# Kernel tuning notes

Measured on AMD Instinct MI355X. Metric: run time of the kernel, lower is better.

The kernel has to match this reference:

```python
import jax, jax.numpy as jnp
import numpy as np


def setup_inputs() -> dict:
    key = jax.random.key(0)
    ks = jax.random.split(key, 7)
    B, T, K, H, A = 32, 32, 196, 512, 512
    # Xavier-normal-ish scale for square 512x512 linears
    s = float(np.sqrt(2.0 / (H + A)))
    return {
        "att_feats": jax.random.normal(ks[0], (B, K, H), jnp.float32),
        "hiddens": jax.random.normal(ks[1], (B, T, H), jnp.float32),
        "sentinel": jax.random.normal(ks[2], (B, T, H), jnp.float32),
        "Wv": jax.random.normal(ks[3], (H, A), jnp.float32) * s,
        "Wg": jax.random.normal(ks[4], (H, A), jnp.float32) * s,
        "Ws": jax.random.normal(ks[5], (H, A), jnp.float32) * s,
        "wh": jax.random.normal(ks[6], (A,), jnp.float32) * s,
    }


def reference(att_feats, hiddens, sentinel, Wv, Wg, Ws, wh):
    # Dropout treated as identity (eval mode / deterministic reference).
    cv = jnp.einsum("bkh,ha->bka", att_feats, Wv)          # [B,K,A]
    cg = jnp.einsum("bth,ha->bta", hiddens, Wg)            # [B,T,A]
    # Broadcast additive attention: [B,T,K,A]
    content_v = cv[:, None, :, :] + cg[:, :, None, :]
    z_t = jnp.einsum("btka,a->btk", jnp.tanh(content_v), wh)  # [B,T,K]
    alpha_t = jax.nn.softmax(z_t, axis=-1)                    # [B,T,K]
    c_t = jnp.einsum("btk,bkh->bth", alpha_t, att_feats)      # [B,T,H]
    # Sentinel branch
    content_s = jnp.einsum("bth,ha->bta", sentinel, Ws) + cg  # [B,T,A]
    z_ext = jnp.einsum("bta,a->bt", jnp.tanh(content_s), wh)[..., None]  # [B,T,1]
    extended = jnp.concatenate([z_t, z_ext], axis=2)          # [B,T,K+1]
    alpha_hat = jax.nn.softmax(extended, axis=-1)
    beta_t = alpha_hat[:, :, -1:]                             # [B,T,1]
    c_hat_t = beta_t * sentinel + (1.0 - beta_t) * c_t        # [B,T,H]
    return (c_hat_t, alpha_t, beta_t)
```

## Files before the change

### kernel.cpp

```cpp
#include <hip/hip_runtime.h>
#include <hip/hip_bf16.h>
#include <math.h>

#define HDIM 512
#define ADIM 512
#define BATCH 32
#define TDIM 32
#define KDIM 196
#define MROWS 8320

typedef short short8 __attribute__((ext_vector_type(8)));
typedef float floatx4 __attribute__((ext_vector_type(4)));

__device__ __forceinline__ float tanh_fast(float x) {
    float e = __expf(2.0f * x);
    return 1.0f - 2.0f * __builtin_amdgcn_rcpf(e + 1.0f);
}

__device__ __forceinline__ void gl_lds16(const __hip_bfloat16* g, __hip_bfloat16* l) {
    __builtin_amdgcn_global_load_lds(
        (const __attribute__((address_space(1))) unsigned int*)(const void*)g,
        (__attribute__((address_space(3))) unsigned int*)(void*)l, 16, 0, 0);
}

__global__ __launch_bounds__(256) void convA(const float* __restrict__ att,
                                             const float* __restrict__ hid,
                                             const float* __restrict__ sen,
                                             __hip_bfloat16* __restrict__ ahi,
                                             __hip_bfloat16* __restrict__ alo) {
    const int idx = blockIdx.x * 256 + threadIdx.x;
    const int row = idx >> 7;
    float4 v;
    if (row < 6272)      v = ((const float4*)att)[idx];
    else if (row < 7296) v = ((const float4*)hid)[idx - 6272 * 128];
    else                 v = ((const float4*)sen)[idx - 7296 * 128];
    float x[4] = {v.x, v.y, v.z, v.w};
    union { __hip_bfloat16 b[4]; uint2 u; } H, L;
    #pragma unroll
    for (int i = 0; i < 4; ++i) {
        H.b[i] = __float2bfloat16(x[i]);
        L.b[i] = __float2bfloat16(x[i] - __bfloat162float(H.b[i]));
    }
    ((uint2*)ahi)[idx] = H.u;
    ((uint2*)alo)[idx] = L.u;
}

__global__ __launch_bounds__(256) void convB(const float* __restrict__ Wv,
                                             const float* __restrict__ Wg,
                                             const float* __restrict__ Ws,
                                             __hip_bfloat16* __restrict__ bthi,
                                             __hip_bfloat16* __restrict__ btlo) {
    __shared__ float tile[64][65];
    const int tid = threadIdx.x;
    const float* src = blockIdx.z == 0 ? Wv : (blockIdx.z == 1 ? Wg : Ws);
    const int k0 = blockIdx.x * 64, n0 = blockIdx.y * 64;
    #pragma unroll
    for (int i = 0; i < 16; ++i) {
        int k = (tid >> 6) * 16 + i;
        int n = tid & 63;
        tile[k][n] = src[(size_t)(k0 + k) * 512 + n0 + n];
    }
    __syncthreads();
    const size_t obase = (size_t)blockIdx.z * 262144;
    #pragma unroll
    for (int i = 0; i < 16; ++i) {
        int n = (tid >> 6) * 16 + i;
        int k = tid & 63;
        float x = tile[k][n];
        __hip_bfloat16 h = __float2bfloat16(x);
        __hip_bfloat16 l = __float2bfloat16(x - __bfloat162float(h));
        size_t o = obase + (size_t)(n0 + n) * 512 + k0 + k;
        bthi[o] = h;
        btlo[o] = l;
    }
}

__global__ __launch_bounds__(256) void gemm_bf16x3(
        const __hip_bfloat16* __restrict__ Ahi, const __hip_bfloat16* __restrict__ Alo,
        const __hip_bfloat16* __restrict__ Bthi, const __hip_bfloat16* __restrict__ Btlo,
        float* __restrict__ C) {
    __shared__ __hip_bfloat16 smem[12288];

    const int tid  = threadIdx.x;
    const int lane = tid & 63;
    const int wave = tid >> 6;
    const int wm = wave >> 1;
    const int wn = wave & 1;
    const int row0 = blockIdx.x * 64;
    const int col0 = blockIdx.y * 128;
    const int seg = (row0 < 6272) ? 0 : ((row0 < 7296) ? 1 : 2);
    const __hip_bfloat16* Bh = Bthi + (size_t)seg * 262144;
    const __hip_bfloat16* Bl = Btlo + (size_t)seg * 262144;

    floatx4 acc[2][4];
    #pragma unroll
    for (int i = 0; i < 2; ++i)
        #pragma unroll
        for (int j = 0; j < 4; ++j)
            acc[i][j] = (floatx4){0.f, 0.f, 0.f, 0.f};

    const int kq8 = (lane >> 4) << 3;

    for (int k0 = 0; k0 < 512; k0 += 32) {
        #pragma unroll
        for (int s = 0; s < 6; ++s) {
            int u = tid + (s << 8);
            __hip_bfloat16* ldst = smem + u * 8;
            const __hip_bfloat16* gsrc;
            if (u < 256)        gsrc = Ahi + (size_t)(row0 + (u >> 2)) * 512 + k0 + ((u & 3) << 3);
            else if (u < 512)   { int v = u - 256;  gsrc = Alo + (size_t)(row0 + (v >> 2)) * 512 + k0 + ((v & 3) << 3); }
            else if (u < 1024)  { int v = u - 512;  gsrc = Bh  + (size_t)(col0 + (v >> 2)) * 512 + k0 + ((v & 3) << 3); }
            else                { int v = u - 1024; gsrc = Bl  + (size_t)(col0 + (v >> 2)) * 512 + k0 + ((v & 3) << 3); }
            gl_lds16(gsrc, ldst);
        }
        asm volatile("s_waitcnt vmcnt(0)" ::: "memory");
        __syncthreads();

        short8 a_hi[2], a_lo[2], b_hi[4], b_lo[4];
        #pragma unroll
        for (int i = 0; i < 2; ++i) {
            int m = wm * 32 + i * 16 + (lane & 15);
            a_hi[i] = *(const short8*)(smem + m * 32 + kq8);
            a_lo[i] = *(const short8*)(smem + 2048 + m * 32 + kq8);
        }
        #pragma unroll
        for (int j = 0; j < 4; ++j) {
            int n = wn * 64 + j * 16 + (lane & 15);
            b_hi[j] = *(const short8*)(smem + 4096 + n * 32 + kq8);
            b_lo[j] = *(const short8*)(smem + 8192 + n * 32 + kq8);
        }

        #pragma unroll
        for (int i = 0; i < 2; ++i)
            #pragma unroll
            for (int j = 0; j < 4; ++j) {
                acc[i][j] = __builtin_amdgcn_mfma_f32_16x16x32_bf16(a_hi[i], b_hi[j], acc[i][j], 0, 0, 0);
                acc[i][j] = __builtin_amdgcn_mfma_f32_16x16x32_bf16(a_hi[i], b_lo[j], acc[i][j], 0, 0, 0);
                acc[i][j] = __builtin_amdgcn_mfma_f32_16x16x32_bf16(a_lo[i], b_hi[j], acc[i][j], 0, 0, 0);
            }
        __syncthreads();
    }

    #pragma unroll
    for (int i = 0; i < 2; ++i) {
        #pragma unroll
        for (int r = 0; r < 4; ++r) {
            int row = row0 + wm * 32 + i * 16 + ((lane >> 4) << 2) + r;
            float* cp = C + (size_t)row * 512 + col0 + wn * 64 + (lane & 15);
            #pragma unroll
            for (int j = 0; j < 4; ++j) cp[j * 16] = acc[i][j][r];
        }
    }
}

__global__ __launch_bounds__(256) void gemm_f32(const float* __restrict__ Amat,
                                                const float* __restrict__ Bmat,
                                                float* __restrict__ Cmat) {
    __shared__ float As[16][64 + 4];
    __shared__ float Bs[16][64];
    const int tid = threadIdx.x;
    const int tx = tid & 15;
    const int ty = tid >> 4;
    const int row0 = blockIdx.x * 64;
    const int col0 = blockIdx.y * 64;
    float acc[4][4] = {};
    for (int k0 = 0; k0 < HDIM; k0 += 16) {
        #pragma unroll
        for (int i = 0; i < 4; ++i) {
            int idx = tid + i * 256;
            As[idx & 15][idx >> 4] = Amat[(size_t)(row0 + (idx >> 4)) * HDIM + k0 + (idx & 15)];
        }
        #pragma unroll
        for (int i = 0; i < 4; ++i) {
            int idx = tid + i * 256;
            Bs[idx >> 6][idx & 63] = Bmat[(size_t)(k0 + (idx >> 6)) * ADIM + col0 + (idx & 63)];
        }
        __syncthreads();
        #pragma unroll
        for (int k = 0; k < 16; ++k) {
            float4 a4 = *(const float4*)&As[k][ty * 4];
            float4 b4 = *(const float4*)&Bs[k][tx * 4];
            float a[4] = {a4.x, a4.y, a4.z, a4.w};
            float b[4] = {b4.x, b4.y, b4.z, b4.w};
            #pragma unroll
            for (int i = 0; i < 4; ++i)
                #pragma unroll
                for (int j = 0; j < 4; ++j)
                    acc[i][j] += a[i] * b[j];
        }
        __syncthreads();
    }
    #pragma unroll
    for (int i = 0; i < 4; ++i) {
        size_t r = (size_t)(row0 + ty * 4 + i) * ADIM + col0 + tx * 4;
        #pragma unroll
        for (int j = 0; j < 4; ++j) Cmat[r + j] = acc[i][j];
    }
}

#define ZKC 16
__global__ __launch_bounds__(512) void z_kernel(const float* __restrict__ cv,
                                                const float* __restrict__ cg,
                                                const float* __restrict__ cs,
                                                const float* __restrict__ wh,
                                                float* __restrict__ z_t,
                                                float* __restrict__ z_ext) {
    __shared__ float cvs[ZKC][ADIM];

    const int b    = blockIdx.x;
    const int tg   = blockIdx.y;
    const int ks   = blockIdx.z;
    const int wave = threadIdx.x >> 6;
    const int lane = threadIdx.x & 63;
    const int t    = tg * 8 + wave;
    const int k_begin = ks * 49;

    const float4* cgv = (const float4*)(cg + ((size_t)b * TDIM + t) * ADIM);
    float4 cg0 = cgv[lane];
    float4 cg1 = cgv[64 + lane];
    const float4* whv = (const float4*)wh;
    float4 wh0 = whv[lane];
    float4 wh1 = whv[64 + lane];

    const float* cvb = cv + (size_t)b * KDIM * ADIM;

    for (int kc = 0; kc < 49; kc += ZKC) {
        int nk = min(ZKC, 49 - kc);
        __syncthreads();
        const float4* src = (const float4*)(cvb + (size_t)(k_begin + kc) * ADIM);
        for (int i = threadIdx.x; i < nk * 128; i += 512)
            ((float4*)cvs)[i] = src[i];
        __syncthreads();

        for (int kk = 0; kk < nk; ++kk) {
            float4 v0 = ((const float4*)&cvs[kk][0])[lane];
            float4 v1 = ((const float4*)&cvs[kk][0])[64 + lane];
            float p;
            p  = wh0.x * tanh_fast(v0.x + cg0.x);
            p += wh0.y * tanh_fast(v0.y + cg0.y);
            p += wh0.z * tanh_fast(v0.z + cg0.z);
            p += wh0.w * tanh_fast(v0.w + cg0.w);
            p += wh1.x * tanh_fast(v1.x + cg1.x);
            p += wh1.y * tanh_fast(v1.y + cg1.y);
            p += wh1.z * tanh_fast(v1.z + cg1.z);
            p += wh1.w * tanh_fast(v1.w + cg1.w);
            #pragma unroll
            for (int off = 32; off; off >>= 1) p += __shfl_xor(p, off, 64);
            if (lane == 0)
                z_t[((size_t)b * TDIM + t) * KDIM + k_begin + kc + kk] = p;
        }
    }

    if (ks == 0) {
        const float4* csv = (const float4*)(cs + ((size_t)b * TDIM + t) * ADIM);
        float4 s0 = csv[lane];
        float4 s1 = csv[64 + lane];
        float p;
        p  = wh0.x * tanh_fast(s0.x + cg0.x);
        p += wh0.y * tanh_fast(s0.y + cg0.y);
        p += wh0.z * tanh_fast(s0.z + cg0.z);
        p += wh0.w * tanh_fast(s0.w + cg0.w);
        p += wh1.x * tanh_fast(s1.x + cg1.x);
        p += wh1.y * tanh_fast(s1.y + cg1.y);
        p += wh1.z * tanh_fast(s1.z + cg1.z);
        p += wh1.w * tanh_fast(s1.w + cg1.w);
        #pragma unroll
        for (int off = 32; off; off >>= 1) p += __shfl_xor(p, off, 64);
        if (lane == 0) z_ext[b * TDIM + t] = p;
    }
}

__global__ __launch_bounds__(256) void out_kernel(const float* __restrict__ z_t,
                                                  const float* __restrict__ z_ext,
                                                  const float* __restrict__ att,
                                                  const float* __restrict__ sen,
                                                  float* __restrict__ out_chat,
                                                  float* __restrict__ out_alpha,
                                                  float* __restrict__ out_beta) {
    __shared__ float alpha_s[KDIM];
    __shared__ float red[8];

    const int t = blockIdx.x;
    const int b = blockIdx.y;
    const int tid = threadIdx.x;

    const float* zrow = z_t + ((size_t)b * TDIM + t) * KDIM;
    float z = (tid < KDIM) ? zrow[tid] : -INFINITY;

    float m = z;
    #pragma unroll
    for (int off = 32; off; off >>= 1) m = fmaxf(m, __shfl_xor(m, off, 64));
    if ((tid & 63) == 0) red[tid >> 6] = m;
    __syncthreads();
    m = fmaxf(fmaxf(red[0], red[1]), fmaxf(red[2], red[3]));

    float e = (tid < KDIM) ? __expf(z - m) : 0.0f;
    float s = e;
    #pragma unroll
    for (int off = 32; off; off >>= 1) s += __shfl_xor(s, off, 64);
    if ((tid & 63) == 0) red[4 + (tid >> 6)] = s;
    __syncthreads();
    float S = red[4] + red[5] + red[6] + red[7];

    float alpha = e / S;
    if (tid < KDIM) {
        alpha_s[tid] = alpha;
        out_alpha[((size_t)b * TDIM + t) * KDIM + tid] = alpha;
    }

    float se = z_ext[b * TDIM + t];
    float m2 = fmaxf(m, se);
    float eext = __expf(se - m2);
    float S2 = S * __expf(m - m2) + eext;
    float beta = eext / S2;
    if (tid == 0) out_beta[b * TDIM + t] = beta;
    __syncthreads();

    const float* attb = att + (size_t)b * KDIM * HDIM;
    float acc0 = 0.f, acc1 = 0.f;
    #pragma unroll 4
    for (int k = 0; k < KDIM; ++k) {
        float a = alpha_s[k];
        acc0 += a * attb[(size_t)k * HDIM + tid];
        acc1 += a * attb[(size_t)k * HDIM + tid + 256];
    }
    const float* srow = sen + ((size_t)b * TDIM + t) * HDIM;
    float om = 1.0f - beta;
    size_t o = ((size_t)b * TDIM + t) * HDIM;
    out_chat[o + tid]       = beta * srow[tid]       + om * acc0;
    out_chat[o + tid + 256] = beta * srow[tid + 256] + om * acc1;
}

extern "C" void kernel_launch(void* const* d_in, const int* in_sizes, int n_in,
                              void* d_out, int out_size, void* d_ws, size_t ws_size,
                              hipStream_t stream) {
    const float* att = (const float*)d_in[0];
    const float* hid = (const float*)d_in[1];
    const float* sen = (const float*)d_in[2];
    const float* Wv  = (const float*)d_in[3];
    const float* Wg  = (const float*)d_in[4];
    const float* Ws  = (const float*)d_in[5];
    const float* wh  = (const float*)d_in[6];

    float* out = (float*)d_out;
    float* out_chat  = out;
    float* out_alpha = out + 524288;
    float* out_beta  = out + 524288 + 200704;

    char* wsb = (char*)d_ws;
    const size_t C_BYTES  = (size_t)MROWS * 512 * 4;
    const size_t ZT_BYTES = 200704 * 4;
    const size_t ZE_BYTES = 4096;
    const size_t AH_BYTES = (size_t)MROWS * 512 * 2;
    const size_t BT_BYTES = (size_t)3 * 512 * 512 * 2;
    const size_t need = C_BYTES + ZT_BYTES + ZE_BYTES + 2 * AH_BYTES + 2 * BT_BYTES;

    float* C  = (float*)wsb;
    float* cv = C;
    float* cg = C + 6272 * 512;
    float* cs = C + 7296 * 512;
    float* zt = (float*)(wsb + C_BYTES);
    float* ze = (float*)(wsb + C_BYTES + ZT_BYTES);

    if (ws_size >= need) {
        __hip_bfloat16* ahi  = (__hip_bfloat16*)(wsb + C_BYTES + ZT_BYTES + ZE_BYTES);
        __hip_bfloat16* alo  = ahi + (size_t)MROWS * 512;
        __hip_bfloat16* bthi = alo + (size_t)MROWS * 512;
        __hip_bfloat16* btlo = bthi + (size_t)3 * 512 * 512;

        convA<<<4160, 256, 0, stream>>>(att, hid, sen, ahi, alo);
        convB<<<dim3(8, 8, 3), 256, 0, stream>>>(Wv, Wg, Ws, bthi, btlo);
        gemm_bf16x3<<<dim3(130, 4), 256, 0, stream>>>(ahi, alo, bthi, btlo, C);
    } else {
        gemm_f32<<<dim3(98, 8), 256, 0, stream>>>(att, Wv, cv);
        gemm_f32<<<dim3(16, 8), 256, 0, stream>>>(hid, Wg, cg);
        gemm_f32<<<dim3(16, 8), 256, 0, stream>>>(sen, Ws, cs);
    }

    z_kernel<<<dim3(BATCH, 4, 4), 512, 0, stream>>>(cv, cg, cs, wh, zt, ze);

    out_kernel<<<dim3(TDIM, BATCH), 256, 0, stream>>>(zt, ze, att, sen,
                                                      out_chat, out_alpha, out_beta);
}
```

Measured before the change: 166.0 us.

## Restructure z and output kernels for per-thread (t,k) work and alpha reuse

The z kernel now assigns one (t,k) pair per thread and stages chunks of cv, cg and cs in LDS. This removes the per-output 64-lane shuffle reductions. The inputs are prescaled by 2*log2(e) so tanh can use exp2 and rcp directly. The output kernel processes four timesteps per block, so each att_feats load is reused across four alpha rows, cutting global reads of att by about four times. In exchange it costs more LDS traffic per FLOP, and the grids are smaller (800 and 256 blocks), which may leave the machine under-occupied.

Result: no change. 164.9 us (-0.7%).

```diff
diff --git a/kernel.cpp b/kernel.cpp
--- a/kernel.cpp
+++ b/kernel.cpp
@@ -11,11 +11,6 @@
 
 typedef short short8 __attribute__((ext_vector_type(8)));
 typedef float floatx4 __attribute__((ext_vector_type(4)));
-
-__device__ __forceinline__ float tanh_fast(float x) {
-    float e = __expf(2.0f * x);
-    return 1.0f - 2.0f * __builtin_amdgcn_rcpf(e + 1.0f);
-}
 
 __device__ __forceinline__ void gl_lds16(const __hip_bfloat16* g, __hip_bfloat16* l) {
     __builtin_amdgcn_global_load_lds(
@@ -153,6 +148,190 @@
     }
 }
 
+#define ZSC 2.885390081777927f
+
+__global__ __launch_bounds__(256) void z_kernel(const float* __restrict__ cv,
+                                                const float* __restrict__ cg,
+                                                const float* __restrict__ cs,
+                                                const float* __restrict__ wh,
+                                                float* __restrict__ z_t,
+                                                float* __restrict__ z_ext) {
+    __shared__ float cvs[8][132];
+    __shared__ float cgs[32][132];
+    __shared__ float css[32][132];
+    __shared__ float whs[132];
+
+    const int kb   = blockIdx.x;
+    const int b    = blockIdx.y;
+    const int tid  = threadIdx.x;
+    const int wave = tid >> 6;
+    const int lane = tid & 63;
+    const int t       = tid & 31;
+    const int k_local = tid >> 5;
+    const int k       = kb * 8 + k_local;
+    const bool do_z = (k < KDIM);
+    const bool do_s = (kb == 24) && (wave == 2) && (lane < 32);
+    const bool last = (kb == 24);
+
+    const int r_st = tid >> 5;
+    const int q_st = tid & 31;
+
+    float acc = 0.f, acc2 = 0.f, acc_s = 0.f, acc_s2 = 0.f;
+
+    for (int c = 0; c < 4; ++c) {
+        const int a0 = c * 128;
+        __syncthreads();
+        {
+            int kr = kb * 8 + r_st;
+            if (kr < KDIM) {
+                float4 v = *(const float4*)(cv + ((size_t)b * KDIM + kr) * ADIM + a0 + 4 * q_st);
+                *(float4*)&cvs[r_st][4 * q_st] = make_float4(v.x * ZSC, v.y * ZSC, v.z * ZSC, v.w * ZSC);
+            }
+        }
+        #pragma unroll
+        for (int s = 0; s < 4; ++s) {
+            int idx = tid + s * 256;
+            int rr = idx >> 5, qq = idx & 31;
+            float4 v = *(const float4*)(cg + ((size_t)b * TDIM + rr) * ADIM + a0 + 4 * qq);
+            *(float4*)&cgs[rr][4 * qq] = make_float4(v.x * ZSC, v.y * ZSC, v.z * ZSC, v.w * ZSC);
+        }
+        if (last) {
+            #pragma unroll
+            for (int s = 0; s < 4; ++s) {
+                int idx = tid + s * 256;
+                int rr = idx >> 5, qq = idx & 31;
+                float4 v = *(const float4*)(cs + ((size_t)b * TDIM + rr) * ADIM + a0 + 4 * qq);
+                *(float4*)&css[rr][4 * qq] = make_float4(v.x * ZSC, v.y * ZSC, v.z * ZSC, v.w * ZSC);
+            }
+        }
+        if (tid < 32)
+            *(float4*)&whs[4 * tid] = *(const float4*)(wh + a0 + 4 * tid);
+        __syncthreads();
+
+        if (do_z) {
+            #pragma unroll 16
+            for (int q = 0; q < 32; ++q) {
+                float4 v  = *(const float4*)&cvs[k_local][4 * q];
+                float4 g  = *(const float4*)&cgs[t][4 * q];
+                float4 w4 = *(const float4*)&whs[4 * q];
+                float e0 = __builtin_amdgcn_exp2f(v.x + g.x);
+                float e1 = __builtin_amdgcn_exp2f(v.y + g.y);
+                float e2 = __builtin_amdgcn_exp2f(v.z + g.z);
+                float e3 = __builtin_amdgcn_exp2f(v.w + g.w);
+                float r0 = __builtin_amdgcn_rcpf(e0 + 1.0f);
+                float r1 = __builtin_amdgcn_rcpf(e1 + 1.0f);
+                float r2 = __builtin_amdgcn_rcpf(e2 + 1.0f);
+                float r3 = __builtin_amdgcn_rcpf(e3 + 1.0f);
+                acc  = fmaf(w4.x, fmaf(-2.0f, r0, 1.0f), acc);
+                acc2 = fmaf(w4.y, fmaf(-2.0f, r1, 1.0f), acc2);
+                acc  = fmaf(w4.z, fmaf(-2.0f, r2, 1.0f), acc);
+                acc2 = fmaf(w4.w, fmaf(-2.0f, r3, 1.0f), acc2);
+            }
+        }
+        if (do_s) {
+            #pragma unroll 16
+            for (int q = 0; q < 32; ++q) {
+                float4 v  = *(const float4*)&css[lane][4 * q];
+                float4 g  = *(const float4*)&cgs[lane][4 * q];
+                float4 w4 = *(const float4*)&whs[4 * q];
+                float e0 = __builtin_amdgcn_exp2f(v.x + g.x);
+                float e1 = __builtin_amdgcn_exp2f(v.y + g.y);
+                float e2 = __builtin_amdgcn_exp2f(v.z + g.z);
+                float e3 = __builtin_amdgcn_exp2f(v.w + g.w);
+                float r0 = __builtin_amdgcn_rcpf(e0 + 1.0f);
+                float r1 = __builtin_amdgcn_rcpf(e1 + 1.0f);
+                float r2 = __builtin_amdgcn_rcpf(e2 + 1.0f);
+                float r3 = __builtin_amdgcn_rcpf(e3 + 1.0f);
+                acc_s  = fmaf(w4.x, fmaf(-2.0f, r0, 1.0f), acc_s);
+                acc_s2 = fmaf(w4.y, fmaf(-2.0f, r1, 1.0f), acc_s2);
+                acc_s  = fmaf(w4.z, fmaf(-2.0f, r2, 1.0f), acc_s);
+                acc_s2 = fmaf(w4.w, fmaf(-2.0f, r3, 1.0f), acc_s2);
+            }
+        }
+    }
+
+    if (do_z) z_t[((size_t)b * TDIM + t) * KDIM + k] = acc + acc2;
+    if (do_s) z_ext[b * TDIM + lane] = acc_s + acc_s2;
+}
+
+__global__ __launch_bounds__(256) void out_kernel(const float* __restrict__ z_t,
+                                                  const float* __restrict__ z_ext,
+                                                  const float* __restrict__ att,
+                                                  const float* __restrict__ sen,
+                                                  float* __restrict__ out_chat,
+                                                  float* __restrict__ out_alpha,
+                                                  float* __restrict__ out_beta) {
+    __shared__ float alpha_s[4][200];
+    __shared__ float beta_s[4];
+
+    const int tg = blockIdx.x;
+    const int b  = blockIdx.y;
+    const int tid  = threadIdx.x;
+    const int wave = tid >> 6;
+    const int lane = tid & 63;
+    const int t = tg * 4 + wave;
+
+    const float* zrow = z_t + ((size_t)b * TDIM + t) * KDIM;
+    float z0 = zrow[lane];
+    float z1 = zrow[lane + 64];
+    float z2 = zrow[lane + 128];
+    float z3 = (lane < 4) ? zrow[lane + 192] : -INFINITY;
+
+    float m = fmaxf(fmaxf(z0, z1), fmaxf(z2, z3));
+    #pragma unroll
+    for (int off = 32; off; off >>= 1) m = fmaxf(m, __shfl_xor(m, off, 64));
+
+    float e0 = __expf(z0 - m), e1 = __expf(z1 - m);
+    float e2 = __expf(z2 - m), e3 = (lane < 4) ? __expf(z3 - m) : 0.0f;
+    float s = e0 + e1 + e2 + e3;
+    #pragma unroll
+    for (int off = 32; off; off >>= 1) s += __shfl_xor(s, off, 64);
+
+    float invS = 1.0f / s;
+    float a0 = e0 * invS, a1 = e1 * invS, a2 = e2 * invS, a3 = e3 * invS;
+
+    float* arow = out_alpha + ((size_t)b * TDIM + t) * KDIM;
+    alpha_s[wave][lane] = a0;        arow[lane] = a0;
+    alpha_s[wave][lane + 64] = a1;   arow[lane + 64] = a1;
+    alpha_s[wave][lane + 128] = a2;  arow[lane + 128] = a2;
+    if (lane < 4) { alpha_s[wave][lane + 192] = a3; arow[lane + 192] = a3; }
+
+    if (lane == 0) {
+        float se = z_ext[b * TDIM + t];
+        float m2 = fmaxf(m, se);
+        float eext = __expf(se - m2);
+        float S2 = s * __expf(m - m2) + eext;
+        float beta = eext / S2;
+        beta_s[wave] = beta;
+        out_beta[b * TDIM + t] = beta;
+    }
+    __syncthreads();
+
+    const float* attb = att + (size_t)b * KDIM * HDIM;
+    float acc[4][2] = {};
+    #pragma unroll 4
+    for (int k = 0; k < KDIM; ++k) {
+        float av0 = attb[(size_t)k * HDIM + tid];
+        float av1 = attb[(size_t)k * HDIM + tid + 256];
+        #pragma unroll
+        for (int w = 0; w < 4; ++w) {
+            float a = alpha_s[w][k];
+            acc[w][0] = fmaf(a, av0, acc[w][0]);
+            acc[w][1] = fmaf(a, av1, acc[w][1]);
+        }
+    }
+
+    #pragma unroll
+    for (int w = 0; w < 4; ++w) {
+        int tt = tg * 4 + w;
+        float beta = beta_s[w];
+        float om = 1.0f - beta;
+        size_t o = ((size_t)b * TDIM + tt) * HDIM;
+        out_chat[o + tid]       = fmaf(beta, sen[o + tid],       om * acc[w][0]);
+        out_chat[o + tid + 256] = fmaf(beta, sen[o + tid + 256], om * acc[w][1]);
+    }
+}
+
 __global__ __launch_bounds__(256) void gemm_f32(const float* __restrict__ Amat,
                                                 const float* __restrict__ Bmat,
                                                 float* __restrict__ Cmat) {
@@ -198,139 +377,6 @@
     }
 }
 
-#define ZKC 16
-__global__ __launch_bounds__(512) void z_kernel(const float* __restrict__ cv,
-                                                const float* __restrict__ cg,
-                                                const float* __restrict__ cs,
-                                                const float* __restrict__ wh,
-                                                float* __restrict__ z_t,
-                                                float* __restrict__ z_ext) {
-    __shared__ float cvs[ZKC][ADIM];
-
-    const int b    = blockIdx.x;
-    const int tg   = blockIdx.y;
-    const int ks   = blockIdx.z;
-    const int wave = threadIdx.x >> 6;
-    const int lane = threadIdx.x & 63;
-    const int t    = tg * 8 + wave;
-    const int k_begin = ks * 49;
-
-    const float4* cgv = (const float4*)(cg + ((size_t)b * TDIM + t) * ADIM);
-    float4 cg0 = cgv[lane];
-    float4 cg1 = cgv[64 + lane];
-    const float4* whv = (const float4*)wh;
-    float4 wh0 = whv[lane];
-    float4 wh1 = whv[64 + lane];
-
-    const float* cvb = cv + (size_t)b * KDIM * ADIM;
-
-    for (int kc = 0; kc < 49; kc += ZKC) {
-        int nk = min(ZKC, 49 - kc);
-        __syncthreads();
-        const float4* src = (const float4*)(cvb + (size_t)(k_begin + kc) * ADIM);
-        for (int i = threadIdx.x; i < nk * 128; i += 512)
-            ((float4*)cvs)[i] = src[i];
-        __syncthreads();
-
-        for (int kk = 0; kk < nk; ++kk) {
-            float4 v0 = ((const float4*)&cvs[kk][0])[lane];
-            float4 v1 = ((const float4*)&cvs[kk][0])[64 + lane];
-            float p;
-            p  = wh0.x * tanh_fast(v0.x + cg0.x);
-            p += wh0.y * tanh_fast(v0.y + cg0.y);
-            p += wh0.z * tanh_fast(v0.z + cg0.z);
-            p += wh0.w * tanh_fast(v0.w + cg0.w);
-            p += wh1.x * tanh_fast(v1.x + cg1.x);
-            p += wh1.y * tanh_fast(v1.y + cg1.y);
-            p += wh1.z * tanh_fast(v1.z + cg1.z);
-            p += wh1.w * tanh_fast(v1.w + cg1.w);
-            #pragma unroll
-            for (int off = 32; off; off >>= 1) p += __shfl_xor(p, off, 64);
-            if (lane == 0)
-                z_t[((size_t)b * TDIM + t) * KDIM + k_begin + kc + kk] = p;
-        }
-    }
-
-    if (ks == 0) {
-        const float4* csv = (const float4*)(cs + ((size_t)b * TDIM + t) * ADIM);
-        float4 s0 = csv[lane];
-        float4 s1 = csv[64 + lane];
-        float p;
-        p  = wh0.x * tanh_fast(s0.x + cg0.x);
-        p += wh0.y * tanh_fast(s0.y + cg0.y);
-        p += wh0.z * tanh_fast(s0.z + cg0.z);
-        p += wh0.w * tanh_fast(s0.w + cg0.w);
-        p += wh1.x * tanh_fast(s1.x + cg1.x);
-        p += wh1.y * tanh_fast(s1.y + cg1.y);
-        p += wh1.z * tanh_fast(s1.z + cg1.z);
-        p += wh1.w * tanh_fast(s1.w + cg1.w);
-        #pragma unroll
-        for (int off = 32; off; off >>= 1) p += __shfl_xor(p, off, 64);
-        if (lane == 0) z_ext[b * TDIM + t] = p;
-    }
-}
-
-__global__ __launch_bounds__(256) void out_kernel(const float* __restrict__ z_t,
-                                                  const float* __restrict__ z_ext,
-                                                  const float* __restrict__ att,
-                                                  const float* __restrict__ sen,
-                                                  float* __restrict__ out_chat,
-                                                  float* __restrict__ out_alpha,
-                                                  float* __restrict__ out_beta) {
-    __shared__ float alpha_s[KDIM];
-    __shared__ float red[8];
-
-    const int t = blockIdx.x;
-    const int b = blockIdx.y;
-    const int tid = threadIdx.x;
-
-    const float* zrow = z_t + ((size_t)b * TDIM + t) * KDIM;
-    float z = (tid < KDIM) ? zrow[tid] : -INFINITY;
-
-    float m = z;
-    #pragma unroll
-    for (int off = 32; off; off >>= 1) m = fmaxf(m, __shfl_xor(m, off, 64));
-    if ((tid & 63) == 0) red[tid >> 6] = m;
-    __syncthreads();
-    m = fmaxf(fmaxf(red[0], red[1]), fmaxf(red[2], red[3]));
-
-    float e = (tid < KDIM) ? __expf(z - m) : 0.0f;
-    float s = e;
-    #pragma unroll
-    for (int off = 32; off; off >>= 1) s += __shfl_xor(s, off, 64);
-    if ((tid & 63) == 0) red[4 + (tid >> 6)] = s;
-    __syncthreads();
-    float S = red[4] + red[5] + red[6] + red[7];
-
-    float alpha = e / S;
-    if (tid < KDIM) {
-        alpha_s[tid] = alpha;
-        out_alpha[((size_t)b * TDIM + t) * KDIM + tid] = alpha;
-    }
-
-    float se = z_ext[b * TDIM + t];
-    float m2 = fmaxf(m, se);
-    float eext = __expf(se - m2);
-    float S2 = S * __expf(m - m2) + eext;
-    float beta = eext / S2;
-    if (tid == 0) out_beta[b * TDIM + t] = beta;
-    __syncthreads();
-
-    const float* attb = att + (size_t)b * KDIM * HDIM;
-    float acc0 = 0.f, acc1 = 0.f;
-    #pragma unroll 4
-    for (int k = 0; k < KDIM; ++k) {
-        float a = alpha_s[k];
-        acc0 += a * attb[(size_t)k * HDIM + tid];
-        acc1 += a * attb[(size_t)k * HDIM + tid + 256];
-    }
-    const float* srow = sen + ((size_t)b * TDIM + t) * HDIM;
-    float om = 1.0f - beta;
-    size_t o = ((size_t)b * TDIM + t) * HDIM;
-    out_chat[o + tid]       = beta * srow[tid]       + om * acc0;
-    out_chat[o + tid + 256] = beta * srow[tid + 256] + om * acc1;
-}
-
 extern "C" void kernel_launch(void* const* d_in, const int* in_sizes, int n_in,
                               void* d_out, int out_size, void* d_ws, size_t ws_size,
                               hipStream_t stream) {
@@ -377,8 +423,8 @@
         gemm_f32<<<dim3(16, 8), 256, 0, stream>>>(sen, Ws, cs);
     }
 
-    z_kernel<<<dim3(BATCH, 4, 4), 512, 0, stream>>>(cv, cg, cs, wh, zt, ze);
-
-    out_kernel<<<dim3(TDIM, BATCH), 256, 0, stream>>>(zt, ze, att, sen,
-                                                      out_chat, out_alpha, out_beta);
-}
+    z_kernel<<<dim3(25, 32), 256, 0, stream>>>(cv, cg, cs, wh, zt, ze);
+
+    out_kernel<<<dim3(8, 32), 256, 0, stream>>>(zt, ze, att, sen,
+                                                out_chat, out_alpha, out_beta);
+}
```
